# Optimization experiments

Hardware: AMD Instinct MI355X
Metric: run time of the kernel (lower is better)

Reference implementation:

```python
import jax, jax.numpy as jnp
import numpy as np

D_MODEL = 1024
N_HEADS = 16
D_HEAD = D_MODEL // N_HEADS
MEM_SIZE = 256


def setup_inputs() -> dict:
    key = jax.random.key(0)
    k_x, k_q, k_o, k_mk, k_mv = jax.random.split(key, 5)
    B, T = 4, 4096
    x = jax.random.normal(k_x, (B, T, D_MODEL), dtype=jnp.float32)
    # xavier_uniform for square Linear weights: bound = sqrt(6/(fan_in+fan_out))
    bound = float(np.sqrt(6.0 / (D_MODEL + D_MODEL)))
    Wq = jax.random.uniform(k_q, (D_MODEL, D_MODEL), minval=-bound, maxval=bound, dtype=jnp.float32)
    Wo = jax.random.uniform(k_o, (D_MODEL, D_MODEL), minval=-bound, maxval=bound, dtype=jnp.float32)
    # kaiming_uniform(a=sqrt(5)) on (H,S,D): fan_in = S*D (last two dims), bound = sqrt(6/((1+a^2)*fan_in)) = 1/sqrt(fan_in)
    bk = float(1.0 / np.sqrt(MEM_SIZE * D_HEAD))
    M_k = jax.random.uniform(k_mk, (N_HEADS, MEM_SIZE, D_HEAD), minval=-bk, maxval=bk, dtype=jnp.float32)
    M_v = jax.random.uniform(k_mv, (N_HEADS, MEM_SIZE, D_HEAD), minval=-0.01, maxval=0.01, dtype=jnp.float32)
    return {"x": x, "Wq": Wq, "Wo": Wo, "M_k": M_k, "M_v": M_v}


def reference(x, Wq, Wo, M_k, M_v):
    B, T, _ = x.shape
    H, S, D = N_HEADS, MEM_SIZE, D_HEAD
    # Q projection (torch Linear: x @ W^T) -> (B, H, T, D)
    Q = (x @ Wq.T).reshape(B, T, H, D).transpose(0, 2, 1, 3)
    scale = D ** -0.5
    # (B, H, T, S) attention against shared external keys
    attn = jnp.einsum("bhtd,hsd->bhts", Q, M_k) * scale
    attn = jax.nn.softmax(attn, axis=-1)
    # double normalization: L1 over the token (T) axis
    attn = attn / (attn.sum(axis=-2, keepdims=True) + 1e-6)
    # dropout = 0.0 (inference): no-op
    out = jnp.einsum("bhts,hsd->bhtd", attn, M_v)
    out = out.transpose(0, 2, 1, 3).reshape(B, T, H * D)
    return out @ Wo.T
```

## Files before the change

### kernel.cpp

```cpp
#include <hip/hip_runtime.h>
#include <math.h>

constexpr int B_  = 4;
constexpr int T_  = 4096;
constexpr int DM_ = 1024;
constexpr int H_  = 16;
constexpr int S_  = 256;
constexpr int BT_ = B_ * T_;
constexpr int NT_ = T_ / 64;
constexpr size_t QELEMS = (size_t)BT_ * DM_;

typedef _Float16 v8h __attribute__((ext_vector_type(8)));
typedef _Float16 v4h __attribute__((ext_vector_type(4)));
typedef float    v4f __attribute__((ext_vector_type(4)));

__device__ _Float16 g_AH[QELEMS];
__device__ _Float16 g_QH[QELEMS];
__device__ _Float16 g_WqH[DM_ * DM_];
__device__ _Float16 g_WoH[DM_ * DM_];
__device__ _Float16 g_MkH[H_ * S_ * 64];
__device__ _Float16 g_MvT[H_ * 64 * S_];
__device__ _Float16 g_Mv2[(size_t)B_ * H_ * 64 * S_];
__device__ _Float16 g_P[(size_t)B_ * H_ * T_ * S_];
__device__ float    g_cpart[(size_t)B_ * H_ * NT_ * S_];
__device__ float    g_colsum_inv[B_ * H_ * S_];

__global__ __launch_bounds__(256) void cvt_h(const float* __restrict__ src,
                                             _Float16* __restrict__ dst,
                                             float scale) {
  const size_t i = (size_t)blockIdx.x * 256 + threadIdx.x;
  const float4* s = (const float4*)src;
  float4 a = s[2 * i], b = s[2 * i + 1];
  v8h o;
  o[0] = (_Float16)(a.x * scale); o[1] = (_Float16)(a.y * scale);
  o[2] = (_Float16)(a.z * scale); o[3] = (_Float16)(a.w * scale);
  o[4] = (_Float16)(b.x * scale); o[5] = (_Float16)(b.y * scale);
  o[6] = (_Float16)(b.z * scale); o[7] = (_Float16)(b.w * scale);
  *(v8h*)&dst[8 * i] = o;
}

__global__ __launch_bounds__(256) void transpose_mv(const float* __restrict__ Mv) {
  const int idx = blockIdx.x * 256 + threadIdx.x;
  const int h = idx >> 14, rem = idx & 16383;
  const int s = rem >> 6, d = rem & 63;
  g_MvT[h * 16384 + d * 256 + s] = (_Float16)Mv[idx];
}

template <typename OUT_T>
__device__ __forceinline__ void gemm_body(const _Float16* __restrict__ Ah,
                                          const _Float16* __restrict__ Wh,
                                          OUT_T* __restrict__ C, float scale) {
  __shared__ _Float16 As[128][72];
  __shared__ _Float16 Bs[128][72];
  const int tid  = threadIdx.x;
  const int m0   = blockIdx.x * 128;
  const int n0   = blockIdx.y * 128;
  const int wid  = tid >> 6;
  const int wm   = wid & 1;
  const int wn   = wid >> 1;
  const int lane = tid & 63;
  const int l15  = lane & 15;
  const int quad = lane >> 4;

  v4f acc[4][4] = {};

  for (int k0 = 0; k0 < 1024; k0 += 64) {
#pragma unroll
    for (int i = 0; i < 4; ++i) {
      int c  = i * 256 + tid;
      int r  = c >> 3;
      int ch = (c & 7) * 8;
      *(v8h*)&As[r][ch] = *(const v8h*)&Ah[(size_t)(m0 + r) * 1024 + k0 + ch];
      *(v8h*)&Bs[r][ch] = *(const v8h*)&Wh[(size_t)(n0 + r) * 1024 + k0 + ch];
    }
    __syncthreads();
#pragma unroll
    for (int kk = 0; kk < 2; ++kk) {
      v8h af[4], bf[4];
#pragma unroll
      for (int i = 0; i < 4; ++i)
        af[i] = *(const v8h*)&As[wm * 64 + i * 16 + l15][kk * 32 + quad * 8];
#pragma unroll
      for (int j = 0; j < 4; ++j)
        bf[j] = *(const v8h*)&Bs[wn * 64 + j * 16 + l15][kk * 32 + quad * 8];
#pragma unroll
      for (int i = 0; i < 4; ++i)
#pragma unroll
        for (int j = 0; j < 4; ++j)
          acc[i][j] = __builtin_amdgcn_mfma_f32_16x16x32_f16(af[i], bf[j], acc[i][j], 0, 0, 0);
    }
    __syncthreads();
  }
#pragma unroll
  for (int i = 0; i < 4; ++i) {
    const size_t mrow = (size_t)(m0 + wm * 64 + i * 16 + quad * 4);
#pragma unroll
    for (int j = 0; j < 4; ++j) {
      const int ncol = n0 + wn * 64 + j * 16 + l15;
#pragma unroll
      for (int r = 0; r < 4; ++r)
        C[(mrow + r) * 1024 + ncol] = (OUT_T)(acc[i][j][r] * scale);
    }
  }
}

__global__ __launch_bounds__(256) void gemm_q16(const _Float16* __restrict__ Wq) {
  gemm_body<_Float16>(g_AH, Wq, g_QH, 1.0f);
}
__global__ __launch_bounds__(256) void gemm_o(const _Float16* __restrict__ Wo,
                                              float* __restrict__ out) {
  gemm_body<float>(g_AH, Wo, out, 1.0f / 512.0f);
}

__global__ __launch_bounds__(256, 4) void attn_p1() {
  __shared__ __align__(16) _Float16 Psh[64][272];
  __shared__ float csum_sh[4][256];
  const int tid  = threadIdx.x;
  const int bh   = blockIdx.x;
  const int b    = bh >> 4, h = bh & 15;
  const int tile = blockIdx.y;
  const int t0   = tile * 64;
  const int wid  = tid >> 6;
  const int lane = tid & 63;
  const int l15  = lane & 15;
  const int quad = lane >> 4;
  char* MkS = (char*)&Psh[0][0];

  const _Float16* qrow = &g_QH[(size_t)(b * T_ + t0 + wid * 16 + l15) * 1024 + h * 64];
  v8h a0 = *(const v8h*)&qrow[quad * 8];
  v8h a1 = *(const v8h*)&qrow[32 + quad * 8];

  {
    const _Float16* mkrow = &g_MkH[h * (S_ * 64) + tid * 64];
#pragma unroll
    for (int c = 0; c < 8; ++c) {
      v8h v = *(const v8h*)&mkrow[c * 8];
      *(v8h*)(MkS + tid * 128 + ((c ^ (tid & 7)) << 4)) = v;
    }
  }
  __syncthreads();

  v4f acc[16] = {};
#pragma unroll
  for (int st = 0; st < 16; ++st) {
    const int row = st * 16 + l15;
    const int sw  = row & 7;
    v8h b0 = *(const v8h*)(MkS + row * 128 + ((quad ^ sw) << 4));
    v8h b1 = *(const v8h*)(MkS + row * 128 + (((4 + quad) ^ sw) << 4));
    acc[st] = __builtin_amdgcn_mfma_f32_16x16x32_f16(a0, b0, acc[st], 0, 0, 0);
    acc[st] = __builtin_amdgcn_mfma_f32_16x16x32_f16(a1, b1, acc[st], 0, 0, 0);
  }

#pragma unroll
  for (int r = 0; r < 4; ++r) {
    float ssum = 0.0f;
#pragma unroll
    for (int st = 0; st < 16; ++st) {
      float p = __expf(acc[st][r]);
      acc[st][r] = p; ssum += p;
    }
    ssum += __shfl_xor(ssum, 1); ssum += __shfl_xor(ssum, 2);
    ssum += __shfl_xor(ssum, 4); ssum += __shfl_xor(ssum, 8);
    const float inv = 1.0f / ssum;
#pragma unroll
    for (int st = 0; st < 16; ++st) acc[st][r] *= inv;
  }

#pragma unroll
  for (int st = 0; st < 16; ++st) {
    float c = acc[st][0] + acc[st][1] + acc[st][2] + acc[st][3];
    c += __shfl_xor(c, 16);
    c += __shfl_xor(c, 32);
    if (quad == 0) csum_sh[wid][st * 16 + l15] = c;
  }
  __syncthreads();
  g_cpart[((size_t)bh * NT_ + tile) * 256 + tid] =
      csum_sh[0][tid] + csum_sh[1][tid] + csum_sh[2][tid] + csum_sh[3][tid];

#pragma unroll
  for (int st = 0; st < 16; ++st)
#pragma unroll
    for (int r = 0; r < 4; ++r)
      Psh[wid * 16 + quad * 4 + r][st * 16 + l15] = (_Float16)acc[st][r];
  __syncthreads();
  {
    const int rr = tid >> 2, q = tid & 3;
    _Float16* prow = &g_P[((size_t)bh * T_ + t0 + rr) * 256 + q * 64];
#pragma unroll
    for (int j = 0; j < 8; ++j)
      *(v8h*)&prow[j * 8] = *(const v8h*)&Psh[rr][q * 64 + j * 8];
  }
}

__global__ __launch_bounds__(256) void reduce_colsum() {
  const int bh = blockIdx.x;
  const int s  = threadIdx.x;
  float acc = 0.0f;
#pragma unroll 8
  for (int k = 0; k < NT_; ++k)
    acc += g_cpart[((size_t)bh * NT_ + k) * 256 + s];
  g_colsum_inv[bh * 256 + s] = 1.0f / (acc + 1e-6f);
}

__global__ __launch_bounds__(256) void scale_mv() {
  const int i8  = blockIdx.x * 256 + threadIdx.x;
  const int bhd = i8 >> 5;
  const int sc  = (i8 & 31) * 8;
  const int h   = (bhd >> 6) & 15;
  const int d   = bhd & 63;
  const int bh  = bhd >> 6;
  v8h mv = *(const v8h*)&g_MvT[(h * 64 + d) * 256 + sc];
  const float* cinv = &g_colsum_inv[bh * 256 + sc];
  v8h o;
#pragma unroll
  for (int j = 0; j < 8; ++j) o[j] = (_Float16)((float)mv[j] * cinv[j]);
  *(v8h*)&g_Mv2[(size_t)bhd * 256 + sc] = o;
}

__global__ __launch_bounds__(256, 2) void pv2() {
  const int tid  = threadIdx.x;
  const int bh   = blockIdx.x;
  const int b    = bh >> 4, h = bh & 15;
  const int gblk = blockIdx.y;
  const int wid  = tid >> 6;
  const int lane = tid & 63;
  const int l15  = lane & 15;
  const int quad = lane >> 4;

  const _Float16* mv2 = &g_Mv2[(size_t)bh * 16384];
  v8h af[4][8];
#pragma unroll
  for (int nt = 0; nt < 4; ++nt)
#pragma unroll
    for (int kc = 0; kc < 8; ++kc)
      af[nt][kc] = *(const v8h*)&mv2[(nt * 16 + l15) * 256 + kc * 32 + quad * 8];

  const int t0w = gblk * 512 + wid * 128;
  const _Float16* pbase = &g_P[((size_t)bh * T_ + t0w) * 256];
  _Float16* obase = &g_AH[((size_t)(b * T_ + t0w)) * 1024 + h * 64];

  v8h bf[8];
#pragma unroll
  for (int kc = 0; kc < 8; ++kc)
    bf[kc] = *(const v8h*)&pbase[(size_t)l15 * 256 + kc * 32 + quad * 8];

  for (int g = 0; g < 8; ++g) {
    v8h nbf[8];
    if (g < 7) {
#pragma unroll
      for (int kc = 0; kc < 8; ++kc)
        nbf[kc] = *(const v8h*)&pbase[(size_t)((g + 1) * 16 + l15) * 256 + kc * 32 + quad * 8];
    }
    v4f acc[4] = {};
#pragma unroll
    for (int kc = 0; kc < 8; ++kc)
#pragma unroll
      for (int nt = 0; nt < 4; ++nt)
        acc[nt] = __builtin_amdgcn_mfma_f32_16x16x32_f16(af[nt][kc], bf[kc], acc[nt], 0, 0, 0);

    _Float16* orow = &obase[(size_t)(g * 16 + l15) * 1024 + quad * 4];
#pragma unroll
    for (int nt = 0; nt < 4; ++nt) {
      v4h o;
#pragma unroll
      for (int r = 0; r < 4; ++r) o[r] = (_Float16)(acc[nt][r] * 512.0f);
      *(v4h*)&orow[nt * 16] = o;
    }
    if (g < 7) {
#pragma unroll
      for (int kc = 0; kc < 8; ++kc) bf[kc] = nbf[kc];
    }
  }
}

extern "C" void kernel_launch(void* const* d_in, const int* in_sizes, int n_in,
                              void* d_out, int out_size, void* d_ws, size_t ws_size,
                              hipStream_t stream) {
  const float* x  = (const float*)d_in[0];
  const float* Wq = (const float*)d_in[1];
  const float* Wo = (const float*)d_in[2];
  const float* Mk = (const float*)d_in[3];
  const float* Mv = (const float*)d_in[4];
  float* out = (float*)d_out;

  _Float16 *AH, *WqH, *WoH, *MkH;
  (void)hipGetSymbolAddress((void**)&AH,  HIP_SYMBOL(g_AH));
  (void)hipGetSymbolAddress((void**)&WqH, HIP_SYMBOL(g_WqH));
  (void)hipGetSymbolAddress((void**)&WoH, HIP_SYMBOL(g_WoH));
  (void)hipGetSymbolAddress((void**)&MkH, HIP_SYMBOL(g_MkH));

  cvt_h<<<8192, 256, 0, stream>>>(x,  AH, 1.0f);
  cvt_h<<<512,  256, 0, stream>>>(Wq, WqH, 1.0f);
  cvt_h<<<512,  256, 0, stream>>>(Wo, WoH, 1.0f);
  cvt_h<<<128,  256, 0, stream>>>(Mk, MkH, 0.125f);
  transpose_mv<<<1024, 256, 0, stream>>>(Mv);
  gemm_q16<<<dim3(BT_ / 128, DM_ / 128), 256, 0, stream>>>(WqH);
  attn_p1<<<dim3(B_ * H_, NT_), 256, 0, stream>>>();
  reduce_colsum<<<dim3(B_ * H_), 256, 0, stream>>>();
  scale_mv<<<512, 256, 0, stream>>>();
  pv2<<<dim3(B_ * H_, 8), 256, 0, stream>>>();
  gemm_o<<<dim3(BT_ / 128, DM_ / 128), 256, 0, stream>>>(WoH, out);
}
```

Measured before the change: 354.7 us.

## Use direct global-to-LDS loads with XOR swizzle in GEMMs, fuse colsum and Mv scaling

The shared GEMM body now fills LDS with global_load_lds DMA instead of staging through registers, and replaces the padded tiles with an XOR-swizzled layout so MFMA fragment reads avoid bank conflicts. The grid is transposed so consecutive blocks share the same M tile of activations and walk across the weight's N tiles, which should improve L2 reuse of activations. The column-sum reduction and the Mv scaling are merged into one kernel that keeps the inverse sums in shared memory, removing one launch and a global buffer. The swizzle indexing is less obvious and relies on 16-byte global_load_lds support.

```diff
diff --git a/kernel.cpp b/kernel.cpp
--- a/kernel.cpp
+++ b/kernel.cpp
@@ -23,7 +23,6 @@
 __device__ _Float16 g_Mv2[(size_t)B_ * H_ * 64 * S_];
 __device__ _Float16 g_P[(size_t)B_ * H_ * T_ * S_];
 __device__ float    g_cpart[(size_t)B_ * H_ * NT_ * S_];
-__device__ float    g_colsum_inv[B_ * H_ * S_];
 
 __global__ __launch_bounds__(256) void cvt_h(const float* __restrict__ src,
                                              _Float16* __restrict__ dst,
@@ -50,11 +49,11 @@
 __device__ __forceinline__ void gemm_body(const _Float16* __restrict__ Ah,
                                           const _Float16* __restrict__ Wh,
                                           OUT_T* __restrict__ C, float scale) {
-  __shared__ _Float16 As[128][72];
-  __shared__ _Float16 Bs[128][72];
+  __shared__ __align__(16) _Float16 As[128 * 64];
+  __shared__ __align__(16) _Float16 Bs[128 * 64];
   const int tid  = threadIdx.x;
-  const int m0   = blockIdx.x * 128;
-  const int n0   = blockIdx.y * 128;
+  const int n0   = blockIdx.x * 128;
+  const int m0   = blockIdx.y * 128;
   const int wid  = tid >> 6;
   const int wm   = wid & 1;
   const int wn   = wid >> 1;
@@ -62,27 +61,38 @@
   const int l15  = lane & 15;
   const int quad = lane >> 4;
 
+  const int lrow = lane >> 3;
+  const int gc   = (lane & 7) ^ lrow;
+  const _Float16* agp = Ah + (size_t)(m0 + wid * 32 + lrow) * 1024 + gc * 8;
+  const _Float16* bgp = Wh + (size_t)(n0 + wid * 32 + lrow) * 1024 + gc * 8;
+  _Float16* asl = As + wid * 2048;
+  _Float16* bsl = Bs + wid * 2048;
+
   v4f acc[4][4] = {};
 
   for (int k0 = 0; k0 < 1024; k0 += 64) {
 #pragma unroll
-    for (int i = 0; i < 4; ++i) {
-      int c  = i * 256 + tid;
-      int r  = c >> 3;
-      int ch = (c & 7) * 8;
-      *(v8h*)&As[r][ch] = *(const v8h*)&Ah[(size_t)(m0 + r) * 1024 + k0 + ch];
-      *(v8h*)&Bs[r][ch] = *(const v8h*)&Wh[(size_t)(n0 + r) * 1024 + k0 + ch];
+    for (int j = 0; j < 4; ++j) {
+      __builtin_amdgcn_global_load_lds(
+          (const __attribute__((address_space(1))) unsigned int*)(agp + (size_t)j * 8192 + k0),
+          (__attribute__((address_space(3))) unsigned int*)(asl + j * 512),
+          16, 0, 0);
+      __builtin_amdgcn_global_load_lds(
+          (const __attribute__((address_space(1))) unsigned int*)(bgp + (size_t)j * 8192 + k0),
+          (__attribute__((address_space(3))) unsigned int*)(bsl + j * 512),
+          16, 0, 0);
     }
     __syncthreads();
 #pragma unroll
     for (int kk = 0; kk < 2; ++kk) {
       v8h af[4], bf[4];
+      const int chx = (kk * 4 + quad) ^ (l15 & 7);
 #pragma unroll
       for (int i = 0; i < 4; ++i)
-        af[i] = *(const v8h*)&As[wm * 64 + i * 16 + l15][kk * 32 + quad * 8];
+        af[i] = *(const v8h*)&As[(wm * 64 + i * 16 + l15) * 64 + chx * 8];
 #pragma unroll
       for (int j = 0; j < 4; ++j)
-        bf[j] = *(const v8h*)&Bs[wn * 64 + j * 16 + l15][kk * 32 + quad * 8];
+        bf[j] = *(const v8h*)&Bs[(wn * 64 + j * 16 + l15) * 64 + chx * 8];
 #pragma unroll
       for (int i = 0; i < 4; ++i)
 #pragma unroll
@@ -192,29 +202,28 @@
   }
 }
 
-__global__ __launch_bounds__(256) void reduce_colsum() {
+__global__ __launch_bounds__(256) void finish_scale_mv() {
+  __shared__ float cs[256];
   const int bh = blockIdx.x;
+  const int h  = bh & 15;
   const int s  = threadIdx.x;
   float acc = 0.0f;
 #pragma unroll 8
   for (int k = 0; k < NT_; ++k)
     acc += g_cpart[((size_t)bh * NT_ + k) * 256 + s];
-  g_colsum_inv[bh * 256 + s] = 1.0f / (acc + 1e-6f);
-}
-
-__global__ __launch_bounds__(256) void scale_mv() {
-  const int i8  = blockIdx.x * 256 + threadIdx.x;
-  const int bhd = i8 >> 5;
-  const int sc  = (i8 & 31) * 8;
-  const int h   = (bhd >> 6) & 15;
-  const int d   = bhd & 63;
-  const int bh  = bhd >> 6;
-  v8h mv = *(const v8h*)&g_MvT[(h * 64 + d) * 256 + sc];
-  const float* cinv = &g_colsum_inv[bh * 256 + sc];
-  v8h o;
-#pragma unroll
-  for (int j = 0; j < 8; ++j) o[j] = (_Float16)((float)mv[j] * cinv[j]);
-  *(v8h*)&g_Mv2[(size_t)bhd * 256 + sc] = o;
+  cs[s] = 1.0f / (acc + 1e-6f);
+  __syncthreads();
+#pragma unroll
+  for (int t = 0; t < 8; ++t) {
+    const int idx = t * 256 + threadIdx.x;
+    const int d  = idx >> 5;
+    const int sc = (idx & 31) * 8;
+    v8h mv = *(const v8h*)&g_MvT[(h * 64 + d) * 256 + sc];
+    v8h o;
+#pragma unroll
+    for (int j = 0; j < 8; ++j) o[j] = (_Float16)((float)mv[j] * cs[sc + j]);
+    *(v8h*)&g_Mv2[(size_t)bh * 16384 + d * 256 + sc] = o;
+  }
 }
 
 __global__ __launch_bounds__(256, 2) void pv2() {
@@ -294,10 +303,9 @@
   cvt_h<<<512,  256, 0, stream>>>(Wo, WoH, 1.0f);
   cvt_h<<<128,  256, 0, stream>>>(Mk, MkH, 0.125f);
   transpose_mv<<<1024, 256, 0, stream>>>(Mv);
-  gemm_q16<<<dim3(BT_ / 128, DM_ / 128), 256, 0, stream>>>(WqH);
+  gemm_q16<<<dim3(DM_ / 128, BT_ / 128), 256, 0, stream>>>(WqH);
   attn_p1<<<dim3(B_ * H_, NT_), 256, 0, stream>>>();
-  reduce_colsum<<<dim3(B_ * H_), 256, 0, stream>>>();
-  scale_mv<<<512, 256, 0, stream>>>();
+  finish_scale_mv<<<B_ * H_, 256, 0, stream>>>();
   pv2<<<dim3(B_ * H_, 8), 256, 0, stream>>>();
-  gemm_o<<<dim3(BT_ / 128, DM_ / 128), 256, 0, stream>>>(WoH, out);
-}
+  gemm_o<<<dim3(DM_ / 128, BT_ / 128), 256, 0, stream>>>(WoH, out);
+}
```

New measurement: 352.0 us. About the same (-0.8%).
